# Kernel optimization log

Hardware: AMD Instinct MI355X
Metric: run time of the kernel (lower is better)

The kernel has to match this reference:

```python
import jax, jax.numpy as jnp
import numpy as np

T, B, IN, OUT, H = 200, 4096, 4, 4, 100
DEC_STEPS = 30

def setup_inputs() -> dict:
    key = jax.random.key(0)
    ks = jax.random.split(key, 12)
    s = 0.1
    return {
        'inputs':   jax.random.normal(ks[0], (T, B, IN), jnp.float32),
        'W_ih_enc': jax.random.normal(ks[1], (4 * H, IN), jnp.float32) * s,
        'W_hh_enc': jax.random.normal(ks[2], (4 * H, H), jnp.float32) * s,
        'b_ih_enc': jax.random.normal(ks[3], (4 * H,), jnp.float32) * s,
        'b_hh_enc': jax.random.normal(ks[4], (4 * H,), jnp.float32) * s,
        'W_ih_dec': jax.random.normal(ks[5], (4 * H, OUT), jnp.float32) * s,
        'W_hh_dec': jax.random.normal(ks[6], (4 * H, H), jnp.float32) * s,
        'b_ih_dec': jax.random.normal(ks[7], (4 * H,), jnp.float32) * s,
        'b_hh_dec': jax.random.normal(ks[8], (4 * H,), jnp.float32) * s,
        'W_y':      jax.random.normal(ks[9], (OUT, H), jnp.float32) * s,
        'b_y':      jax.random.normal(ks[10], (OUT,), jnp.float32) * s,
    }

def _lstm_cell(x, h, c, W_ih, W_hh, b_ih, b_hh):
    # PyTorch LSTMCell: gates ordered (i, f, g, o)
    gates = x @ W_ih.T + b_ih + h @ W_hh.T + b_hh  # [B, 4H]
    i, f, g, o = jnp.split(gates, 4, axis=-1)
    c_new = jax.nn.sigmoid(f) * c + jax.nn.sigmoid(i) * jnp.tanh(g)
    h_new = jax.nn.sigmoid(o) * jnp.tanh(c_new)
    return h_new, c_new

def reference(inputs, W_ih_enc, W_hh_enc, b_ih_enc, b_hh_enc,
              W_ih_dec, W_hh_dec, b_ih_dec, b_hh_dec, W_y, b_y):
    batch = inputs.shape[1]
    hidden = W_hh_enc.shape[1]
    out_dim = W_y.shape[0]

    # ---- encode: scan LSTMCell over time ----
    def enc_step(carry, x_t):
        h, c = carry
        h, c = _lstm_cell(x_t, h, c, W_ih_enc, W_hh_enc, b_ih_enc, b_hh_enc)
        return (h, c), None
    h0 = jnp.zeros((batch, hidden), inputs.dtype)
    c0 = jnp.zeros((batch, hidden), inputs.dtype)
    (h_enc, _), _ = jax.lax.scan(enc_step, (h0, c0), inputs)

    def dec_step(carry, _):
        h, c, y_prev = carry
        h, c = _lstm_cell(y_prev, h, c, W_ih_dec, W_hh_dec, b_ih_dec, b_hh_dec)
        y = h @ W_y.T + b_y
        return (h, c, y), y
    y0 = jnp.zeros((batch, out_dim), inputs.dtype)
    c_dec0 = jnp.zeros((batch, hidden), inputs.dtype)
    _, result = jax.lax.scan(dec_step, (h_enc, c_dec0, y0), None, length=DEC_STEPS)
    return result  # [30, B, OUT]
```

## Files before the change

kernel.cpp:

```cpp
#include <hip/hip_runtime.h>


#define NTHREADS 512
#define NBLOCKS  512
#define BR       8

typedef __attribute__((ext_vector_type(8))) short short8;
typedef __attribute__((ext_vector_type(4))) float f32x4;

#define FRAG_ELEMS 51200
#define BIAS_BYTE_OFF 204800
#define L2E 1.4426950408889634f

__device__ __forceinline__ unsigned short f2bf(float f) {
    unsigned int u = __float_as_uint(f);
    return (unsigned short)((u + 0x7fff + ((u >> 16) & 1)) >> 16);
}
__device__ __forceinline__ float bf2f(unsigned short s) {
    return __uint_as_float(((unsigned int)s) << 16);
}
__device__ __forceinline__ float ex2(float x) {
    float r; asm("v_exp_f32 %0, %1" : "=v"(r) : "v"(x)); return r;
}
__device__ __forceinline__ float rcpf_(float x) { return __builtin_amdgcn_rcpf(x); }

__device__ __forceinline__ float cellup(const f32x4 g, float& c) {
    float si = rcpf_(1.f + ex2(g[0]));
    float sf = rcpf_(1.f + ex2(g[1]));
    float tg = fmaf(-2.f, rcpf_(1.f + ex2(g[2])), 1.f);
    float so = rcpf_(1.f + ex2(g[3]));
    c = fmaf(sf, c, si * tg);
    float tc = fmaf(-2.f, rcpf_(1.f + ex2(c * (2.f * L2E))), 1.f);
    return so * tc;
}

__global__ void prep_kernel(const float* __restrict__ Wih_e, const float* __restrict__ Whh_e,
                            const float* __restrict__ bih_e, const float* __restrict__ bhh_e,
                            const float* __restrict__ Wih_d, const float* __restrict__ Whh_d,
                            const float* __restrict__ bih_d, const float* __restrict__ bhh_d,
                            void* __restrict__ ws)
{
    unsigned short* frag = (unsigned short*)ws;
    float* bias = (float*)((char*)ws + BIAS_BYTE_OFF);
    int gid = blockIdx.x * blockDim.x + threadIdx.x;
    int gsz = gridDim.x * blockDim.x;
    for (int i = gid; i < 2 * FRAG_ELEMS; i += gsz) {
        int which = i / FRAG_ELEMS;
        int e = i - which * FRAG_ELEMS;
        int j8 = e & 7, lane = (e >> 3) & 63, s = (e >> 9) & 3, t = e >> 11;
        int k = s * 32 + (lane >> 4) * 8 + j8;
        int n = t * 16 + (lane & 15);
        int jcol = n >> 2, gate = n & 3, col = gate * 100 + jcol;
        float scale = (gate == 2) ? (2.f * L2E) : -L2E;
        const float* Whh = which ? Whh_d : Whh_e;
        const float* Wih = which ? Wih_d : Wih_e;
        float v = 0.f;
        if (k < 100)      v = Whh[col * 100 + k];
        else if (k < 104) v = Wih[col * 4 + (k - 100)];
        frag[i] = f2bf(v * scale);
    }
    for (int i = gid; i < 800; i += gsz) {
        int which = i / 400, n = i - which * 400;
        int jcol = n >> 2, gate = n & 3, col = gate * 100 + jcol;
        float scale = (gate == 2) ? (2.f * L2E) : -L2E;
        bias[i] = scale * (which ? (bih_d[col] + bhh_d[col]) : (bih_e[col] + bhh_e[col]));
    }
}

__global__ __launch_bounds__(NTHREADS)
__attribute__((amdgpu_waves_per_eu(4, 4)))
void seq2seq_kernel(
    const float* __restrict__ inputs,
    const void* __restrict__ ws,
    const float* __restrict__ Wy,
    const float* __restrict__ by_g,
    float* __restrict__ out)
{
    __shared__ unsigned short A_frag[2048];
    __shared__ float G_lds[BR * 404];
    __shared__ float Wy_lds[404];
    __shared__ unsigned short xstage[6400];

    const unsigned short* fragE = (const unsigned short*)ws;
    const unsigned short* fragD = fragE + FRAG_ELEMS;
    const float* biasE = (const float*)((const char*)ws + BIAS_BYTE_OFF);
    const float* biasD = biasE + 400;

    const int tid = threadIdx.x;
    const int wid = tid >> 6;
    const int wl  = tid & 63;
    const int m   = wl & 15;
    const int q   = wl >> 4;
    const int blk = blockIdx.x;

    for (int i = tid; i < 2048; i += NTHREADS) A_frag[i] = 0;

    for (int i = tid; i < 6400; i += NTHREADS) {
        int s = i >> 5, u = i & 31;
        xstage[i] = f2bf(inputs[((size_t)s * 4096 + blk * BR + (u >> 2)) * 4 + (u & 3)]);
    }

    const int cr = tid & 7, jp = tid >> 3;
    const int j0 = 2 * jp;
    const bool isc = (tid < 400);
    float cst[2] = {0.f, 0.f};

    const bool isx = (tid >= 480);
    const int xu = tid - 480;
    const int xr = xu >> 2, xc = xu & 3;
    const int xelem = (192 + xr) * 8 + 4 + xc;

    short8 bfr[3][4]; float breg[3];
    short8 bfr24[4];  float breg24 = 0.f;
    #pragma unroll
    for (int i = 0; i < 3; ++i) {
        int t = wid + 8 * i;
        #pragma unroll
        for (int s = 0; s < 4; ++s)
            bfr[i][s] = *(const short8*)&fragE[((t * 4 + s) * 64 + wl) * 8];
        breg[i] = biasE[t * 16 + m];
    }
    if (wid == 7) {
        #pragma unroll
        for (int s = 0; s < 4; ++s)
            bfr24[s] = *(const short8*)&fragE[((24 * 4 + s) * 64 + wl) * 8];
        breg24 = biasE[24 * 16 + m];
    }

    __syncthreads();
    if (isx) A_frag[xelem] = xstage[xu];

    for (int step = 0; step < 200; ++step) {
        __syncthreads();
        short8 af[4];
        #pragma unroll
        for (int s = 0; s < 4; ++s)
            af[s] = *(const short8*)&A_frag[(s * 64 + wl) * 8];
        #pragma unroll
        for (int i = 0; i < 3; ++i) {
            int t = wid + 8 * i;
            f32x4 acc = {breg[i], breg[i], breg[i], breg[i]};
            #pragma unroll
            for (int s = 0; s < 4; ++s)
                acc = __builtin_amdgcn_mfma_f32_16x16x32_bf16(af[s], bfr[i][s], acc, 0, 0, 0);
            if (q < 2) {
                #pragma unroll
                for (int r = 0; r < 4; ++r)
                    G_lds[(q * 4 + r) * 404 + t * 16 + m] = acc[r];
            }
        }
        if (wid == 7) {
            f32x4 acc = {breg24, breg24, breg24, breg24};
            #pragma unroll
            for (int s = 0; s < 4; ++s)
                acc = __builtin_amdgcn_mfma_f32_16x16x32_bf16(af[s], bfr24[s], acc, 0, 0, 0);
            if (q < 2) {
                #pragma unroll
                for (int r = 0; r < 4; ++r)
                    G_lds[(q * 4 + r) * 404 + 24 * 16 + m] = acc[r];
            }
        }
        __syncthreads();
        if (isc) {
            f32x4 ga = *(const f32x4*)&G_lds[cr * 404 + 8 * jp];
            f32x4 gb = *(const f32x4*)&G_lds[cr * 404 + 8 * jp + 4];
            float h0 = cellup(ga, cst[0]);
            float h1 = cellup(gb, cst[1]);
            unsigned int pk;
            asm("v_cvt_pk_bf16_f32 %0, %1, %2" : "=v"(pk) : "v"(h0), "v"(h1));
            *(unsigned int*)&A_frag[((j0 >> 3) * 16 + cr) * 8 + (j0 & 7)] = pk;
        }
        if (isx && step < 199)
            A_frag[xelem] = xstage[(step + 1) * 32 + xu];
    }

    #pragma unroll
    for (int i = 0; i < 3; ++i) {
        int t = wid + 8 * i;
        #pragma unroll
        for (int s = 0; s < 4; ++s)
            bfr[i][s] = *(const short8*)&fragD[((t * 4 + s) * 64 + wl) * 8];
        breg[i] = biasD[t * 16 + m];
    }
    if (wid == 7) {
        #pragma unroll
        for (int s = 0; s < 4; ++s)
            bfr24[s] = *(const short8*)&fragD[((24 * 4 + s) * 64 + wl) * 8];
        breg24 = biasD[24 * 16 + m];
    }
    cst[0] = cst[1] = 0.f;
    if (isx) A_frag[xelem] = 0;
    for (int i = tid; i < 404; i += NTHREADS)
        Wy_lds[i] = (i < 400) ? Wy[i] : by_g[i - 400];

    const int yrow = tid >> 5, yln = tid & 31;
    const bool isy = (tid < 256);

    for (int step = 0; step < 30; ++step) {
        __syncthreads();
        short8 af[4];
        #pragma unroll
        for (int s = 0; s < 4; ++s)
            af[s] = *(const short8*)&A_frag[(s * 64 + wl) * 8];
        #pragma unroll
        for (int i = 0; i < 3; ++i) {
            int t = wid + 8 * i;
            f32x4 acc = {breg[i], breg[i], breg[i], breg[i]};
            #pragma unroll
            for (int s = 0; s < 4; ++s)
                acc = __builtin_amdgcn_mfma_f32_16x16x32_bf16(af[s], bfr[i][s], acc, 0, 0, 0);
            if (q < 2) {
                #pragma unroll
                for (int r = 0; r < 4; ++r)
                    G_lds[(q * 4 + r) * 404 + t * 16 + m] = acc[r];
            }
        }
        if (wid == 7) {
            f32x4 acc = {breg24, breg24, breg24, breg24};
            #pragma unroll
            for (int s = 0; s < 4; ++s)
                acc = __builtin_amdgcn_mfma_f32_16x16x32_bf16(af[s], bfr24[s], acc, 0, 0, 0);
            if (q < 2) {
                #pragma unroll
                for (int r = 0; r < 4; ++r)
                    G_lds[(q * 4 + r) * 404 + 24 * 16 + m] = acc[r];
            }
        }
        __syncthreads();
        if (isc) {
            f32x4 ga = *(const f32x4*)&G_lds[cr * 404 + 8 * jp];
            f32x4 gb = *(const f32x4*)&G_lds[cr * 404 + 8 * jp + 4];
            float h0 = cellup(ga, cst[0]);
            float h1 = cellup(gb, cst[1]);
            unsigned int pk;
            asm("v_cvt_pk_bf16_f32 %0, %1, %2" : "=v"(pk) : "v"(h0), "v"(h1));
            *(unsigned int*)&A_frag[((j0 >> 3) * 16 + cr) * 8 + (j0 & 7)] = pk;
        }
        __syncthreads();
        if (isy) {
            float p0 = 0.f, p1 = 0.f, p2 = 0.f, p3 = 0.f;
            #pragma unroll
            for (int i = 0; i < 4; ++i) {
                int j = yln + 32 * i;
                if (j < 100) {
                    float hv = bf2f(A_frag[((j >> 3) * 16 + yrow) * 8 + (j & 7)]);
                    p0 = fmaf(Wy_lds[0 * 100 + j], hv, p0);
                    p1 = fmaf(Wy_lds[1 * 100 + j], hv, p1);
                    p2 = fmaf(Wy_lds[2 * 100 + j], hv, p2);
                    p3 = fmaf(Wy_lds[3 * 100 + j], hv, p3);
                }
            }
            #pragma unroll
            for (int mm = 16; mm >= 1; mm >>= 1) {
                p0 += __shfl_xor(p0, mm, 32);
                p1 += __shfl_xor(p1, mm, 32);
                p2 += __shfl_xor(p2, mm, 32);
                p3 += __shfl_xor(p3, mm, 32);
            }
            if (yln == 0) {
                float y0 = p0 + Wy_lds[400], y1 = p1 + Wy_lds[401];
                float y2 = p2 + Wy_lds[402], y3 = p3 + Wy_lds[403];
                float4 yv = make_float4(y0, y1, y2, y3);
                *(float4*)&out[((size_t)step * 4096 + blk * BR + yrow) * 4] = yv;
                unsigned int pk01, pk23;
                asm("v_cvt_pk_bf16_f32 %0, %1, %2" : "=v"(pk01) : "v"(y0), "v"(y1));
                asm("v_cvt_pk_bf16_f32 %0, %1, %2" : "=v"(pk23) : "v"(y2), "v"(y3));
                *(unsigned int*)&A_frag[(192 + yrow) * 8 + 4] = pk01;
                *(unsigned int*)&A_frag[(192 + yrow) * 8 + 6] = pk23;
            }
        }
    }
}

extern "C" void kernel_launch(void* const* d_in, const int* in_sizes, int n_in,
                              void* d_out, int out_size, void* d_ws, size_t ws_size,
                              hipStream_t stream)
{
    (void)in_sizes; (void)n_in; (void)out_size; (void)ws_size;
    const float* inputs = (const float*)d_in[0];
    const float* Wih_e  = (const float*)d_in[1];
    const float* Whh_e  = (const float*)d_in[2];
    const float* bih_e  = (const float*)d_in[3];
    const float* bhh_e  = (const float*)d_in[4];
    const float* Wih_d  = (const float*)d_in[5];
    const float* Whh_d  = (const float*)d_in[6];
    const float* bih_d  = (const float*)d_in[7];
    const float* bhh_d  = (const float*)d_in[8];
    const float* Wy     = (const float*)d_in[9];
    const float* by     = (const float*)d_in[10];
    float* out = (float*)d_out;

    hipLaunchKernelGGL(prep_kernel, dim3(256), dim3(256), 0, stream,
                       Wih_e, Whh_e, bih_e, bhh_e, Wih_d, Whh_d, bih_d, bhh_d, d_ws);
    hipLaunchKernelGGL(seq2seq_kernel, dim3(NBLOCKS), dim3(NTHREADS), 0, stream,
                       inputs, d_ws, Wy, by, out);
}
```

Measured before the change: 257.6 us.

## Interleave two independent row groups per block to overlap MFMA with cell updates

Each block now handles 16 batch rows as two independent groups of 8, each with its own double-buffered A_frag and G_lds. The MFMA gate computation for one group runs in the same barrier phase as the elementwise cell update for the other, so one barrier separates the stages instead of two per encoder step. The grid shrinks to 256 blocks and the occupancy hint relaxes to 2 waves per EU. Inputs are staged with float4 loads and packed bf16 conversion. The cost is fewer blocks in flight, more LDS per block, and a decoder loop that now has more barriers per step.

```diff
diff --git a/kernel.cpp b/kernel.cpp
--- a/kernel.cpp
+++ b/kernel.cpp
@@ -2,15 +2,14 @@
 
 
 #define NTHREADS 512
-#define NBLOCKS  512
-#define BR       8
+#define NBLOCKS  256
+#define L2E 1.4426950408889634f
 
 typedef __attribute__((ext_vector_type(8))) short short8;
 typedef __attribute__((ext_vector_type(4))) float f32x4;
 
 #define FRAG_ELEMS 51200
 #define BIAS_BYTE_OFF 204800
-#define L2E 1.4426950408889634f
 
 __device__ __forceinline__ unsigned short f2bf(float f) {
     unsigned int u = __float_as_uint(f);
@@ -68,7 +67,7 @@
 }
 
 __global__ __launch_bounds__(NTHREADS)
-__attribute__((amdgpu_waves_per_eu(4, 4)))
+__attribute__((amdgpu_waves_per_eu(2)))
 void seq2seq_kernel(
     const float* __restrict__ inputs,
     const void* __restrict__ ws,
@@ -76,10 +75,10 @@
     const float* __restrict__ by_g,
     float* __restrict__ out)
 {
-    __shared__ unsigned short A_frag[2048];
-    __shared__ float G_lds[BR * 404];
+    __shared__ unsigned short A_frag[2][2048];
+    __shared__ float G_lds[2][8 * 404];
+    __shared__ unsigned short xstage[200 * 64];
     __shared__ float Wy_lds[404];
-    __shared__ unsigned short xstage[6400];
 
     const unsigned short* fragE = (const unsigned short*)ws;
     const unsigned short* fragD = fragE + FRAG_ELEMS;
@@ -93,22 +92,27 @@
     const int q   = wl >> 4;
     const int blk = blockIdx.x;
 
-    for (int i = tid; i < 2048; i += NTHREADS) A_frag[i] = 0;
-
-    for (int i = tid; i < 6400; i += NTHREADS) {
-        int s = i >> 5, u = i & 31;
-        xstage[i] = f2bf(inputs[((size_t)s * 4096 + blk * BR + (u >> 2)) * 4 + (u & 3)]);
-    }
-
-    const int cr = tid & 7, jp = tid >> 3;
-    const int j0 = 2 * jp;
+    for (int i = tid; i < 4096; i += NTHREADS) (&A_frag[0][0])[i] = 0;
+
+    for (int i = tid; i < 200 * 16; i += NTHREADS) {
+        int s = i >> 4, u4 = i & 15;
+        float4 v = *(const float4*)&inputs[((size_t)s * 4096 + blk * 16 + u4) * 4];
+        unsigned int pk01, pk23;
+        asm("v_cvt_pk_bf16_f32 %0, %1, %2" : "=v"(pk01) : "v"(v.x), "v"(v.y));
+        asm("v_cvt_pk_bf16_f32 %0, %1, %2" : "=v"(pk23) : "v"(v.z), "v"(v.w));
+        *(unsigned int*)&xstage[s * 64 + u4 * 4]     = pk01;
+        *(unsigned int*)&xstage[s * 64 + u4 * 4 + 2] = pk23;
+    }
+
+    const int cr = tid & 7, jp = tid >> 3, j0 = 2 * jp;
     const bool isc = (tid < 400);
-    float cst[2] = {0.f, 0.f};
-
-    const bool isx = (tid >= 480);
-    const int xu = tid - 480;
-    const int xr = xu >> 2, xc = xu & 3;
-    const int xelem = (192 + xr) * 8 + 4 + xc;
+    float cst0[2] = {0.f, 0.f}, cst1[2] = {0.f, 0.f};
+
+    const bool isx = (tid >= 448);
+    const int xu = tid - 448;
+    const int xg = xu >> 5;
+    const int xrl = (xu >> 2) & 7, xc = xu & 3;
+    const int xelem = (192 + xrl) * 8 + 4 + xc;
 
     short8 bfr[3][4]; float breg[3];
     short8 bfr24[4];  float breg24 = 0.f;
@@ -127,123 +131,58 @@
         breg24 = biasE[24 * 16 + m];
     }
 
-    __syncthreads();
-    if (isx) A_frag[xelem] = xstage[xu];
-
-    for (int step = 0; step < 200; ++step) {
-        __syncthreads();
+    auto do_mfma = [&](const unsigned short* Ab, float* Gb) {
         short8 af[4];
         #pragma unroll
-        for (int s = 0; s < 4; ++s)
-            af[s] = *(const short8*)&A_frag[(s * 64 + wl) * 8];
+        for (int s4 = 0; s4 < 4; ++s4)
+            af[s4] = *(const short8*)&Ab[(s4 * 64 + wl) * 8];
         #pragma unroll
         for (int i = 0; i < 3; ++i) {
             int t = wid + 8 * i;
             f32x4 acc = {breg[i], breg[i], breg[i], breg[i]};
             #pragma unroll
-            for (int s = 0; s < 4; ++s)
-                acc = __builtin_amdgcn_mfma_f32_16x16x32_bf16(af[s], bfr[i][s], acc, 0, 0, 0);
+            for (int s4 = 0; s4 < 4; ++s4)
+                acc = __builtin_amdgcn_mfma_f32_16x16x32_bf16(af[s4], bfr[i][s4], acc, 0, 0, 0);
             if (q < 2) {
                 #pragma unroll
                 for (int r = 0; r < 4; ++r)
-                    G_lds[(q * 4 + r) * 404 + t * 16 + m] = acc[r];
+                    Gb[(q * 4 + r) * 404 + t * 16 + m] = acc[r];
             }
         }
         if (wid == 7) {
             f32x4 acc = {breg24, breg24, breg24, breg24};
             #pragma unroll
-            for (int s = 0; s < 4; ++s)
-                acc = __builtin_amdgcn_mfma_f32_16x16x32_bf16(af[s], bfr24[s], acc, 0, 0, 0);
+            for (int s4 = 0; s4 < 4; ++s4)
+                acc = __builtin_amdgcn_mfma_f32_16x16x32_bf16(af[s4], bfr24[s4], acc, 0, 0, 0);
             if (q < 2) {
                 #pragma unroll
                 for (int r = 0; r < 4; ++r)
-                    G_lds[(q * 4 + r) * 404 + 24 * 16 + m] = acc[r];
-            }
-        }
-        __syncthreads();
+                    Gb[(q * 4 + r) * 404 + 24 * 16 + m] = acc[r];
+            }
+        }
+    };
+
+    auto do_trans = [&](const float* Gb, unsigned short* Ab, float* cs) {
         if (isc) {
-            f32x4 ga = *(const f32x4*)&G_lds[cr * 404 + 8 * jp];
-            f32x4 gb = *(const f32x4*)&G_lds[cr * 404 + 8 * jp + 4];
-            float h0 = cellup(ga, cst[0]);
-            float h1 = cellup(gb, cst[1]);
+            f32x4 ga = *(const f32x4*)&Gb[cr * 404 + 8 * jp];
+            f32x4 gb = *(const f32x4*)&Gb[cr * 404 + 8 * jp + 4];
+            float h0 = cellup(ga, cs[0]);
+            float h1 = cellup(gb, cs[1]);
             unsigned int pk;
             asm("v_cvt_pk_bf16_f32 %0, %1, %2" : "=v"(pk) : "v"(h0), "v"(h1));
-            *(unsigned int*)&A_frag[((j0 >> 3) * 16 + cr) * 8 + (j0 & 7)] = pk;
-        }
-        if (isx && step < 199)
-            A_frag[xelem] = xstage[(step + 1) * 32 + xu];
-    }
-
-    #pragma unroll
-    for (int i = 0; i < 3; ++i) {
-        int t = wid + 8 * i;
-        #pragma unroll
-        for (int s = 0; s < 4; ++s)
-            bfr[i][s] = *(const short8*)&fragD[((t * 4 + s) * 64 + wl) * 8];
-        breg[i] = biasD[t * 16 + m];
-    }
-    if (wid == 7) {
-        #pragma unroll
-        for (int s = 0; s < 4; ++s)
-            bfr24[s] = *(const short8*)&fragD[((24 * 4 + s) * 64 + wl) * 8];
-        breg24 = biasD[24 * 16 + m];
-    }
-    cst[0] = cst[1] = 0.f;
-    if (isx) A_frag[xelem] = 0;
-    for (int i = tid; i < 404; i += NTHREADS)
-        Wy_lds[i] = (i < 400) ? Wy[i] : by_g[i - 400];
-
-    const int yrow = tid >> 5, yln = tid & 31;
-    const bool isy = (tid < 256);
-
-    for (int step = 0; step < 30; ++step) {
-        __syncthreads();
-        short8 af[4];
-        #pragma unroll
-        for (int s = 0; s < 4; ++s)
-            af[s] = *(const short8*)&A_frag[(s * 64 + wl) * 8];
-        #pragma unroll
-        for (int i = 0; i < 3; ++i) {
-            int t = wid + 8 * i;
-            f32x4 acc = {breg[i], breg[i], breg[i], breg[i]};
-            #pragma unroll
-            for (int s = 0; s < 4; ++s)
-                acc = __builtin_amdgcn_mfma_f32_16x16x32_bf16(af[s], bfr[i][s], acc, 0, 0, 0);
-            if (q < 2) {
-                #pragma unroll
-                for (int r = 0; r < 4; ++r)
-                    G_lds[(q * 4 + r) * 404 + t * 16 + m] = acc[r];
-            }
-        }
-        if (wid == 7) {
-            f32x4 acc = {breg24, breg24, breg24, breg24};
-            #pragma unroll
-            for (int s = 0; s < 4; ++s)
-                acc = __builtin_amdgcn_mfma_f32_16x16x32_bf16(af[s], bfr24[s], acc, 0, 0, 0);
-            if (q < 2) {
-                #pragma unroll
-                for (int r = 0; r < 4; ++r)
-                    G_lds[(q * 4 + r) * 404 + 24 * 16 + m] = acc[r];
-            }
-        }
-        __syncthreads();
-        if (isc) {
-            f32x4 ga = *(const f32x4*)&G_lds[cr * 404 + 8 * jp];
-            f32x4 gb = *(const f32x4*)&G_lds[cr * 404 + 8 * jp + 4];
-            float h0 = cellup(ga, cst[0]);
-            float h1 = cellup(gb, cst[1]);
-            unsigned int pk;
-            asm("v_cvt_pk_bf16_f32 %0, %1, %2" : "=v"(pk) : "v"(h0), "v"(h1));
-            *(unsigned int*)&A_frag[((j0 >> 3) * 16 + cr) * 8 + (j0 & 7)] = pk;
-        }
-        __syncthreads();
-        if (isy) {
+            *(unsigned int*)&Ab[((j0 >> 3) * 16 + cr) * 8 + (j0 & 7)] = pk;
+        }
+    };
+
+    auto do_yproj = [&](unsigned short* Ab, int g, int d) {
+        if (tid < 256) {
+            int yrow = tid >> 5, yln = tid & 31;
             float p0 = 0.f, p1 = 0.f, p2 = 0.f, p3 = 0.f;
             #pragma unroll
             for (int i = 0; i < 4; ++i) {
                 int j = yln + 32 * i;
                 if (j < 100) {
-                    float hv = bf2f(A_frag[((j >> 3) * 16 + yrow) * 8 + (j & 7)]);
+                    float hv = bf2f(Ab[((j >> 3) * 16 + yrow) * 8 + (j & 7)]);
                     p0 = fmaf(Wy_lds[0 * 100 + j], hv, p0);
                     p1 = fmaf(Wy_lds[1 * 100 + j], hv, p1);
                     p2 = fmaf(Wy_lds[2 * 100 + j], hv, p2);
@@ -260,16 +199,68 @@
             if (yln == 0) {
                 float y0 = p0 + Wy_lds[400], y1 = p1 + Wy_lds[401];
                 float y2 = p2 + Wy_lds[402], y3 = p3 + Wy_lds[403];
-                float4 yv = make_float4(y0, y1, y2, y3);
-                *(float4*)&out[((size_t)step * 4096 + blk * BR + yrow) * 4] = yv;
+                *(float4*)&out[((size_t)d * 4096 + blk * 16 + g * 8 + yrow) * 4] =
+                    make_float4(y0, y1, y2, y3);
                 unsigned int pk01, pk23;
                 asm("v_cvt_pk_bf16_f32 %0, %1, %2" : "=v"(pk01) : "v"(y0), "v"(y1));
                 asm("v_cvt_pk_bf16_f32 %0, %1, %2" : "=v"(pk23) : "v"(y2), "v"(y3));
-                *(unsigned int*)&A_frag[(192 + yrow) * 8 + 4] = pk01;
-                *(unsigned int*)&A_frag[(192 + yrow) * 8 + 6] = pk23;
-            }
-        }
-    }
+                *(unsigned int*)&Ab[(192 + yrow) * 8 + 4] = pk01;
+                *(unsigned int*)&Ab[(192 + yrow) * 8 + 6] = pk23;
+            }
+        }
+    };
+
+    __syncthreads();
+    if (isx && xg == 0) A_frag[0][xelem] = xstage[xu];
+    __syncthreads();
+
+    for (int s = 0; s < 200; ++s) {
+        do_mfma(A_frag[0], G_lds[0]);
+        if (s) do_trans(G_lds[1], A_frag[1], cst1);
+        if (isx && xg == 1) A_frag[1][xelem] = xstage[s * 64 + xu];
+        __syncthreads();
+        do_mfma(A_frag[1], G_lds[1]);
+        do_trans(G_lds[0], A_frag[0], cst0);
+        if (isx && xg == 0 && s < 199) A_frag[0][xelem] = xstage[(s + 1) * 64 + xu];
+        __syncthreads();
+    }
+    do_trans(G_lds[1], A_frag[1], cst1);
+
+    #pragma unroll
+    for (int i = 0; i < 3; ++i) {
+        int t = wid + 8 * i;
+        #pragma unroll
+        for (int s = 0; s < 4; ++s)
+            bfr[i][s] = *(const short8*)&fragD[((t * 4 + s) * 64 + wl) * 8];
+        breg[i] = biasD[t * 16 + m];
+    }
+    if (wid == 7) {
+        #pragma unroll
+        for (int s = 0; s < 4; ++s)
+            bfr24[s] = *(const short8*)&fragD[((24 * 4 + s) * 64 + wl) * 8];
+        breg24 = biasD[24 * 16 + m];
+    }
+    cst0[0] = cst0[1] = cst1[0] = cst1[1] = 0.f;
+    if (isx) A_frag[xg][xelem] = 0;
+    for (int i = tid; i < 404; i += NTHREADS)
+        Wy_lds[i] = (i < 400) ? Wy[i] : by_g[i - 400];
+    __syncthreads();
+
+    for (int d = 0; d < 30; ++d) {
+        do_mfma(A_frag[0], G_lds[0]);
+        if (d) do_trans(G_lds[1], A_frag[1], cst1);
+        __syncthreads();
+        if (d) do_yproj(A_frag[1], 1, d - 1);
+        __syncthreads();
+        do_mfma(A_frag[1], G_lds[1]);
+        do_trans(G_lds[0], A_frag[0], cst0);
+        __syncthreads();
+        do_yproj(A_frag[0], 0, d);
+        __syncthreads();
+    }
+    do_trans(G_lds[1], A_frag[1], cst1);
+    __syncthreads();
+    do_yproj(A_frag[1], 1, 29);
 }
 
 extern "C" void kernel_launch(void* const* d_in, const int* in_sizes, int n_in,
```

Result: slower. 317.6 us (+23.3%).

## Process 16 batch rows per block to fill all MFMA rows

Applied to the files above, without the earlier changes.

Each block now handles 16 batch rows instead of 8, using 1024 threads and 16 waves across 256 blocks. Previously half of each 16x16 MFMA tile's rows were padding and their results were thrown away (q<2 guard); now every row is a real batch element, so total MFMA work is halved. Each wave computes at most 2 gate tiles per step instead of 3-4, which shortens the per-step critical path. Input staging is also vectorised with float4 loads and packed bf16 conversion. The trade-off is larger block-wide barriers over 16 waves and only one block per CU, which leaves less overlap between blocks.

```diff
diff --git a/kernel.cpp b/kernel.cpp
--- a/kernel.cpp
+++ b/kernel.cpp
@@ -1,9 +1,9 @@
 #include <hip/hip_runtime.h>
 
 
-#define NTHREADS 512
-#define NBLOCKS  512
-#define BR       8
+#define NTHREADS 1024
+#define NBLOCKS  256
+#define BR       16
 
 typedef __attribute__((ext_vector_type(8))) short short8;
 typedef __attribute__((ext_vector_type(4))) float f32x4;
@@ -67,8 +67,7 @@
     }
 }
 
-__global__ __launch_bounds__(NTHREADS)
-__attribute__((amdgpu_waves_per_eu(4, 4)))
+__global__ __launch_bounds__(NTHREADS, 4)
 void seq2seq_kernel(
     const float* __restrict__ inputs,
     const void* __restrict__ ws,
@@ -79,7 +78,7 @@
     __shared__ unsigned short A_frag[2048];
     __shared__ float G_lds[BR * 404];
     __shared__ float Wy_lds[404];
-    __shared__ unsigned short xstage[6400];
+    __shared__ unsigned short xstage[200 * 64];
 
     const unsigned short* fragE = (const unsigned short*)ws;
     const unsigned short* fragD = fragE + FRAG_ELEMS;
@@ -95,36 +94,35 @@
 
     for (int i = tid; i < 2048; i += NTHREADS) A_frag[i] = 0;
 
-    for (int i = tid; i < 6400; i += NTHREADS) {
-        int s = i >> 5, u = i & 31;
-        xstage[i] = f2bf(inputs[((size_t)s * 4096 + blk * BR + (u >> 2)) * 4 + (u & 3)]);
-    }
-
-    const int cr = tid & 7, jp = tid >> 3;
-    const int j0 = 2 * jp;
-    const bool isc = (tid < 400);
+    for (int i = tid; i < 200 * 16; i += NTHREADS) {
+        int s = i >> 4, u4 = i & 15;
+        float4 v = *(const float4*)&inputs[((size_t)s * 4096 + blk * BR + u4) * 4];
+        unsigned int pk01, pk23;
+        asm("v_cvt_pk_bf16_f32 %0, %1, %2" : "=v"(pk01) : "v"(v.x), "v"(v.y));
+        asm("v_cvt_pk_bf16_f32 %0, %1, %2" : "=v"(pk23) : "v"(v.z), "v"(v.w));
+        *(unsigned int*)&xstage[i * 4]     = pk01;
+        *(unsigned int*)&xstage[i * 4 + 2] = pk23;
+    }
+
+    const int cr = tid & 15, jp = tid >> 4, j0 = 2 * jp;
+    const bool isc = (tid < 800);
     float cst[2] = {0.f, 0.f};
 
-    const bool isx = (tid >= 480);
-    const int xu = tid - 480;
+    const bool isx = (tid >= 960);
+    const int xu = tid - 960;
     const int xr = xu >> 2, xc = xu & 3;
     const int xelem = (192 + xr) * 8 + 4 + xc;
 
-    short8 bfr[3][4]; float breg[3];
-    short8 bfr24[4];  float breg24 = 0.f;
+    short8 bfr[2][4]; float breg[2] = {0.f, 0.f};
     #pragma unroll
-    for (int i = 0; i < 3; ++i) {
-        int t = wid + 8 * i;
-        #pragma unroll
-        for (int s = 0; s < 4; ++s)
-            bfr[i][s] = *(const short8*)&fragE[((t * 4 + s) * 64 + wl) * 8];
-        breg[i] = biasE[t * 16 + m];
-    }
-    if (wid == 7) {
-        #pragma unroll
-        for (int s = 0; s < 4; ++s)
-            bfr24[s] = *(const short8*)&fragE[((24 * 4 + s) * 64 + wl) * 8];
-        breg24 = biasE[24 * 16 + m];
+    for (int i = 0; i < 2; ++i) {
+        int t = wid + 16 * i;
+        if (t < 25) {
+            #pragma unroll
+            for (int s = 0; s < 4; ++s)
+                bfr[i][s] = *(const short8*)&fragE[((t * 4 + s) * 64 + wl) * 8];
+            breg[i] = biasE[t * 16 + m];
+        }
     }
 
     __syncthreads();
@@ -137,27 +135,16 @@
         for (int s = 0; s < 4; ++s)
             af[s] = *(const short8*)&A_frag[(s * 64 + wl) * 8];
         #pragma unroll
-        for (int i = 0; i < 3; ++i) {
-            int t = wid + 8 * i;
-            f32x4 acc = {breg[i], breg[i], breg[i], breg[i]};
-            #pragma unroll
-            for (int s = 0; s < 4; ++s)
-                acc = __builtin_amdgcn_mfma_f32_16x16x32_bf16(af[s], bfr[i][s], acc, 0, 0, 0);
-            if (q < 2) {
+        for (int i = 0; i < 2; ++i) {
+            int t = wid + 16 * i;
+            if (t < 25) {
+                f32x4 acc = {breg[i], breg[i], breg[i], breg[i]};
+                #pragma unroll
+                for (int s = 0; s < 4; ++s)
+                    acc = __builtin_amdgcn_mfma_f32_16x16x32_bf16(af[s], bfr[i][s], acc, 0, 0, 0);
                 #pragma unroll
                 for (int r = 0; r < 4; ++r)
                     G_lds[(q * 4 + r) * 404 + t * 16 + m] = acc[r];
-            }
-        }
-        if (wid == 7) {
-            f32x4 acc = {breg24, breg24, breg24, breg24};
-            #pragma unroll
-            for (int s = 0; s < 4; ++s)
-                acc = __builtin_amdgcn_mfma_f32_16x16x32_bf16(af[s], bfr24[s], acc, 0, 0, 0);
-            if (q < 2) {
-                #pragma unroll
-                for (int r = 0; r < 4; ++r)
-                    G_lds[(q * 4 + r) * 404 + 24 * 16 + m] = acc[r];
             }
         }
         __syncthreads();
@@ -171,22 +158,18 @@
             *(unsigned int*)&A_frag[((j0 >> 3) * 16 + cr) * 8 + (j0 & 7)] = pk;
         }
         if (isx && step < 199)
-            A_frag[xelem] = xstage[(step + 1) * 32 + xu];
+            A_frag[xelem] = xstage[(step + 1) * 64 + xu];
     }
 
     #pragma unroll
-    for (int i = 0; i < 3; ++i) {
-        int t = wid + 8 * i;
-        #pragma unroll
-        for (int s = 0; s < 4; ++s)
-            bfr[i][s] = *(const short8*)&fragD[((t * 4 + s) * 64 + wl) * 8];
-        breg[i] = biasD[t * 16 + m];
-    }
-    if (wid == 7) {
-        #pragma unroll
-        for (int s = 0; s < 4; ++s)
-            bfr24[s] = *(const short8*)&fragD[((24 * 4 + s) * 64 + wl) * 8];
-        breg24 = biasD[24 * 16 + m];
+    for (int i = 0; i < 2; ++i) {
+        int t = wid + 16 * i;
+        if (t < 25) {
+            #pragma unroll
+            for (int s = 0; s < 4; ++s)
+                bfr[i][s] = *(const short8*)&fragD[((t * 4 + s) * 64 + wl) * 8];
+            breg[i] = biasD[t * 16 + m];
+        }
     }
     cst[0] = cst[1] = 0.f;
     if (isx) A_frag[xelem] = 0;
@@ -194,7 +177,7 @@
         Wy_lds[i] = (i < 400) ? Wy[i] : by_g[i - 400];
 
     const int yrow = tid >> 5, yln = tid & 31;
-    const bool isy = (tid < 256);
+    const bool isy = (tid < 512);
 
     for (int step = 0; step < 30; ++step) {
         __syncthreads();
@@ -203,27 +186,16 @@
         for (int s = 0; s < 4; ++s)
             af[s] = *(const short8*)&A_frag[(s * 64 + wl) * 8];
         #pragma unroll
-        for (int i = 0; i < 3; ++i) {
-            int t = wid + 8 * i;
-            f32x4 acc = {breg[i], breg[i], breg[i], breg[i]};
-            #pragma unroll
-            for (int s = 0; s < 4; ++s)
-                acc = __builtin_amdgcn_mfma_f32_16x16x32_bf16(af[s], bfr[i][s], acc, 0, 0, 0);
-            if (q < 2) {
+        for (int i = 0; i < 2; ++i) {
+            int t = wid + 16 * i;
+            if (t < 25) {
+                f32x4 acc = {breg[i], breg[i], breg[i], breg[i]};
+                #pragma unroll
+                for (int s = 0; s < 4; ++s)
+                    acc = __builtin_amdgcn_mfma_f32_16x16x32_bf16(af[s], bfr[i][s], acc, 0, 0, 0);
                 #pragma unroll
                 for (int r = 0; r < 4; ++r)
                     G_lds[(q * 4 + r) * 404 + t * 16 + m] = acc[r];
-            }
-        }
-        if (wid == 7) {
-            f32x4 acc = {breg24, breg24, breg24, breg24};
-            #pragma unroll
-            for (int s = 0; s < 4; ++s)
-                acc = __builtin_amdgcn_mfma_f32_16x16x32_bf16(af[s], bfr24[s], acc, 0, 0, 0);
-            if (q < 2) {
-                #pragma unroll
-                for (int r = 0; r < 4; ++r)
-                    G_lds[(q * 4 + r) * 404 + 24 * 16 + m] = acc[r];
             }
         }
         __syncthreads();
```

Result: faster. 243.1 us (-5.6%).
